# Kernel optimization log

Hardware: AMD Instinct MI355X
Metric: run time of the kernel (lower is better)

The kernel has to match this reference:

```python
import jax, jax.numpy as jnp
import numpy as np

NEG_SLOPE = 0.2


def gatv2_layer(x, edge_index, Wl, Wr, att, bias):
    """PyG GATv2Conv (share_weights=False, concat=True, negative_slope=0.2).
    x: [N, F]; Wl/Wr: [F, H*C]; att: [H, C]; bias: [H*C]. Returns [N, H*C]."""
    N = x.shape[0]
    H, C = att.shape
    src, dst = edge_index[0], edge_index[1]
    xl = (x @ Wl).reshape(N, H, C)  # source transform
    xr = (x @ Wr).reshape(N, H, C)  # target transform
    # per-edge attention logits
    e = jax.nn.leaky_relu(xl[src] + xr[dst], NEG_SLOPE)          # [E, H, C]
    logits = jnp.einsum('ehc,hc->eh', e, att)                     # [E, H]
    # segment softmax over incoming edges of each destination node
    m = jax.ops.segment_max(logits, dst, num_segments=N)          # [N, H]
    m = jnp.where(jnp.isfinite(m), m, 0.0)                        # empty segments
    ex = jnp.exp(logits - m[dst])                                 # [E, H]
    denom = jax.ops.segment_sum(ex, dst, num_segments=N)          # [N, H]
    alpha = ex / (denom[dst] + 1e-16)                             # [E, H]
    msg = xl[src] * alpha[..., None]                              # [E, H, C]
    out = jax.ops.segment_sum(msg, dst, num_segments=N)           # [N, H, C]
    return out.reshape(N, H * C) + bias


def setup_inputs() -> dict:
    key = jax.random.key(0)
    ks = jax.random.split(key, 10)
    N, E, F, H, C, OUT = 50000, 800000, 256, 8, 32, 64
    s = 0.05
    return {
        'x': jax.random.normal(ks[0], (N, F), dtype=jnp.float32),
        'edge_index': jax.random.randint(ks[1], (2, E), 0, N, dtype=jnp.int64),
        'Wl1': jax.random.normal(ks[2], (F, H * C), dtype=jnp.float32) * s,
        'Wr1': jax.random.normal(ks[3], (F, H * C), dtype=jnp.float32) * s,
        'att1': jax.random.normal(ks[4], (H, C), dtype=jnp.float32) * s,
        'b1': jax.random.normal(ks[5], (H * C,), dtype=jnp.float32) * s,
        'Wl2': jax.random.normal(ks[6], (H * C, OUT), dtype=jnp.float32) * s,
        'Wr2': jax.random.normal(ks[7], (H * C, OUT), dtype=jnp.float32) * s,
        'att2': jax.random.normal(ks[8], (1, OUT), dtype=jnp.float32) * s,
        'b2': jax.random.normal(ks[9], (OUT,), dtype=jnp.float32) * s,
    }


def reference(x, edge_index, Wl1, Wr1, att1, b1, Wl2, Wr2, att2, b2):
    h = gatv2_layer(x, edge_index, Wl1, Wr1, att1, b1)
    h = jax.nn.relu(h)
    h = gatv2_layer(h, edge_index, Wl2, Wr2, att2, b2)
    return (h, jax.nn.log_softmax(h, axis=1))
```

## Files before the change

### kernel.cpp

```cpp
#include <hip/hip_runtime.h>
#include <hip/hip_bf16.h>
#include <math.h>

#define NEG_SLOPE 0.2f

typedef __attribute__((ext_vector_type(8))) short short8;
typedef __attribute__((ext_vector_type(4))) float floatx4;
typedef __attribute__((ext_vector_type(2))) float floatx2;

__device__ inline ushort f2b(float f) {
    __hip_bfloat16 b = __float2bfloat16(f);
    return *(ushort*)&b;
}
__device__ inline float b2f(ushort u) {
    union { unsigned int i; float f; } c;
    c.i = ((unsigned int)u) << 16;
    return c.f;
}
__device__ inline floatx2 bf2x2(unsigned int d) {
    union { unsigned int i; float f; } lo, hi;
    lo.i = d << 16;
    hi.i = d & 0xffff0000u;
    floatx2 r = {lo.f, hi.f};
    return r;
}

template<int BM, int BN, typename AT>
__global__ __launch_bounds__(256) void gemm_bf16(const AT* __restrict__ A,
                                                 const ushort* __restrict__ Bt,
                                                 ushort* __restrict__ C,
                                                 int M, int N, int K)
{
    constexpr int SA = 40;
    constexpr int WTM = (BN == 64) ? 32 : 64;
    constexpr int WM  = BM / WTM;
    constexpr int IT  = WTM / 16;
    constexpr int JT  = 4;
    __shared__ ushort As[BM * SA];
    __shared__ ushort Bs[BN * SA];
    const int tid = threadIdx.x;
    const int w = tid >> 6, lane = tid & 63;
    const int mw = (w % WM) * WTM;
    const int nw = (w / WM) * 64;
    const int m0 = blockIdx.y * BM;
    const int n0 = blockIdx.x * BN;
    const int lm = lane & 15;
    const int kg = lane >> 4;

    floatx4 acc[IT][JT];
#pragma unroll
    for (int i = 0; i < IT; ++i)
#pragma unroll
        for (int j = 0; j < JT; ++j) acc[i][j] = (floatx4)0.f;

    for (int k0 = 0; k0 < K; k0 += 32) {
#pragma unroll
        for (int it = 0; it < BM / 64; ++it) {
            int idx = it * 256 + tid;
            int row = idx >> 2, kc = idx & 3;
            int grow = m0 + row;
            if (grow >= M) grow = M - 1;
            if constexpr (sizeof(AT) == 4) {
                float4 f0 = *(const float4*)&A[(size_t)grow * K + k0 + kc * 8];
                float4 f1 = *(const float4*)&A[(size_t)grow * K + k0 + kc * 8 + 4];
                ushort* d = &As[row * SA + kc * 8];
                d[0] = f2b(f0.x); d[1] = f2b(f0.y); d[2] = f2b(f0.z); d[3] = f2b(f0.w);
                d[4] = f2b(f1.x); d[5] = f2b(f1.y); d[6] = f2b(f1.z); d[7] = f2b(f1.w);
            } else {
                short8 v = *(const short8*)&A[(size_t)grow * K + k0 + kc * 8];
                *(short8*)&As[row * SA + kc * 8] = v;
            }
        }
#pragma unroll
        for (int it = 0; it < BN / 64; ++it) {
            int idx = it * 256 + tid;
            int row = idx >> 2, kc = idx & 3;
            short8 v = *(const short8*)&Bt[(size_t)(n0 + row) * K + k0 + kc * 8];
            *(short8*)&Bs[row * SA + kc * 8] = v;
        }
        __syncthreads();
        short8 a[IT], b[JT];
#pragma unroll
        for (int i = 0; i < IT; ++i)
            a[i] = *(const short8*)&As[(mw + i * 16 + lm) * SA + kg * 8];
#pragma unroll
        for (int j = 0; j < JT; ++j)
            b[j] = *(const short8*)&Bs[(nw + j * 16 + lm) * SA + kg * 8];
#pragma unroll
        for (int i = 0; i < IT; ++i)
#pragma unroll
            for (int j = 0; j < JT; ++j)
                acc[i][j] = __builtin_amdgcn_mfma_f32_16x16x32_bf16(a[i], b[j], acc[i][j], 0, 0, 0);
        __syncthreads();
    }

#pragma unroll
    for (int i = 0; i < IT; ++i) {
        int rbase = m0 + mw + i * 16 + (lane >> 4) * 4;
#pragma unroll
        for (int j = 0; j < JT; ++j) {
            int col = n0 + nw + j * 16 + lm;
#pragma unroll
            for (int r = 0; r < 4; ++r) {
                int row = rbase + r;
                if (row < M) C[(size_t)row * N + col] = f2b(acc[i][j][r]);
            }
        }
    }
}

__global__ void k_prep(const float* __restrict__ Wl1, const float* __restrict__ Wr1,
                       const float* __restrict__ Wl2, const float* __restrict__ Wr2,
                       ushort* __restrict__ wlr1t, ushort* __restrict__ wlr2t,
                       const int* __restrict__ dst, int E, int* __restrict__ counts)
{
    const int b = blockIdx.x;
    const int t = threadIdx.x;
    if (b < 640) {
        int i = b * 256 + t;
        if (i < 65536) {
            int k = i >> 8, n = i & 255;
            wlr1t[n * 256 + k] = f2b(Wl1[i]);
        } else if (i < 131072) {
            int j = i - 65536;
            int k = j >> 8, n = j & 255;
            wlr1t[65536 + n * 256 + k] = f2b(Wr1[j]);
        } else if (i < 147456) {
            int j = i - 131072;
            int k = j >> 6, n = j & 63;
            wlr2t[n * 256 + k] = f2b(Wl2[j]);
        } else {
            int j = i - 147456;
            int k = j >> 6, n = j & 63;
            wlr2t[16384 + n * 256 + k] = f2b(Wr2[j]);
        }
    } else {
        int i = (b - 640) * 256 + t;
        if (i < E) atomicAdd(&counts[dst[i]], 1);
    }
}

__global__ void k_chunksum(const int* __restrict__ counts, int N, int* __restrict__ chunk)
{
    __shared__ int sm[256];
    const int t = threadIdx.x;
    const int base = blockIdx.x * 1024;
    int s = 0;
    for (int i = t; i < 1024; i += 256) {
        int idx = base + i;
        s += (idx < N) ? counts[idx] : 0;
    }
    sm[t] = s;
    __syncthreads();
    for (int off = 128; off; off >>= 1) {
        if (t < off) sm[t] += sm[t + off];
        __syncthreads();
    }
    if (t == 0) chunk[blockIdx.x] = sm[0];
}

__global__ void k_scanchunk(int* __restrict__ chunk, int nchunks)
{
    if (blockIdx.x == 0 && threadIdx.x == 0) {
        int run = 0;
        for (int i = 0; i < nchunks; ++i) {
            int c = chunk[i];
            chunk[i] = run;
            run += c;
        }
        chunk[nchunks] = run;
    }
}

__global__ void k_scanwrite(const int* __restrict__ counts, int N,
                            const int* __restrict__ chunk,
                            int* __restrict__ offsets, int* __restrict__ cursor)
{
    __shared__ int sm[256];
    const int t = threadIdx.x;
    const int base = blockIdx.x * 1024 + t * 4;
    int v[4];
    int s = 0;
#pragma unroll
    for (int i = 0; i < 4; ++i) {
        v[i] = (base + i < N) ? counts[base + i] : 0;
        s += v[i];
    }
    sm[t] = s;
    __syncthreads();
    for (int off = 1; off < 256; off <<= 1) {
        int y = (t >= off) ? sm[t - off] : 0;
        __syncthreads();
        sm[t] += y;
        __syncthreads();
    }
    int run = chunk[blockIdx.x] + sm[t] - s;
#pragma unroll
    for (int i = 0; i < 4; ++i) {
        if (base + i < N) {
            offsets[base + i] = run;
            cursor[base + i] = run;
        }
        run += v[i];
    }
    if (blockIdx.x == 0 && t == 0) offsets[N] = chunk[gridDim.x];
}

__global__ void k_fill(const int* __restrict__ src, const int* __restrict__ dst,
                       int E, int* __restrict__ cursor, int* __restrict__ csr_src)
{
    int i = blockIdx.x * blockDim.x + threadIdx.x;
    if (i < E) {
        int d = dst[i];
        int pos = atomicAdd(&cursor[d], 1);
        csr_src[pos] = src[i];
    }
}

__global__ __launch_bounds__(256) void agg1(const ushort* __restrict__ xlr,
                                            const float* __restrict__ att,
                                            const float* __restrict__ bias,
                                            const int* __restrict__ offsets,
                                            const int* __restrict__ csr_src,
                                            ushort* __restrict__ h1, int N)
{
    const int wave = blockIdx.x * 4 + (threadIdx.x >> 6);
    const int lane = threadIdx.x & 63;
    if (wave >= N) return;
    const int n = wave;
    const int g = lane >> 5;
    const int sl = lane & 31;
    const int elem = (sl >> 2) * 32 + (sl & 3) * 8;

    floatx2 attv2[4], xrv2[4];
    {
        uint4 xr8 = *(const uint4*)&xlr[(size_t)n * 512 + 256 + elem];
        unsigned int xw[4] = {xr8.x, xr8.y, xr8.z, xr8.w};
#pragma unroll
        for (int i = 0; i < 4; ++i) {
            attv2[i] = *(const floatx2*)&att[elem + 2 * i];
            xrv2[i] = bf2x2(xw[i]);
        }
    }
    float m = -1e30f, l = 0.f;
    floatx2 acc2[4] = {(floatx2)0.f, (floatx2)0.f, (floatx2)0.f, (floatx2)0.f};

    const int beg = offsets[n], end = offsets[n + 1];
    if (beg < end) {
        uint4 xv;
        {
            int k0 = beg + g;
            int ks = (k0 < end) ? k0 : end - 1;
            xv = *(const uint4*)&xlr[(size_t)csr_src[ks] * 512 + elem];
        }
        for (int kb = beg; kb < end; kb += 2) {
            const int kk = kb + g;
            uint4 cur = xv;
            {
                int kn = kk + 2;
                int ks = (kn < end) ? kn : end - 1;
                xv = *(const uint4*)&xlr[(size_t)csr_src[ks] * 512 + elem];
            }
            if (kk < end) {
                unsigned int cw[4] = {cur.x, cur.y, cur.z, cur.w};
                floatx2 xl2[4];
                floatx2 u2 = (floatx2)0.f;
#pragma unroll
                for (int i = 0; i < 4; ++i) {
                    xl2[i] = bf2x2(cw[i]);
                    floatx2 t = xl2[i] + xrv2[i];
                    t = __builtin_elementwise_max(t, t * NEG_SLOPE);
                    u2 += t * attv2[i];
                }
                float u = u2.x + u2.y;
                u += __shfl_xor(u, 1);
                u += __shfl_xor(u, 2);
                float e = __expf(-fabsf(u - m));
                bool kp = (m >= u);
                float sc = kp ? 1.f : e;
                float p  = kp ? e : 1.f;
                m = fmaxf(m, u);
#pragma unroll
                for (int i = 0; i < 4; ++i) acc2[i] = acc2[i] * sc + xl2[i] * p;
                l = fmaf(l, sc, p);
            }
        }
    }
    {
        float mo = __shfl_xor(m, 32);
        float lo = __shfl_xor(l, 32);
        float nm = fmaxf(m, mo);
        float ea = __expf(m - nm);
        float eb = __expf(mo - nm);
#pragma unroll
        for (int i = 0; i < 4; ++i) {
            floatx2 ao = {__shfl_xor(acc2[i].x, 32), __shfl_xor(acc2[i].y, 32)};
            acc2[i] = acc2[i] * ea + ao * eb;
        }
        l = l * ea + lo * eb;
    }
    if (g == 0) {
        float rl = 1.f / (l + 1e-16f);
        short8 o;
#pragma unroll
        for (int i = 0; i < 4; ++i) {
            float v0 = fmaf(acc2[i].x, rl, bias[elem + 2 * i]);
            float v1 = fmaf(acc2[i].y, rl, bias[elem + 2 * i + 1]);
            o[2 * i]     = (short)f2b(fmaxf(v0, 0.f));
            o[2 * i + 1] = (short)f2b(fmaxf(v1, 0.f));
        }
        *(short8*)&h1[(size_t)n * 256 + elem] = o;
    }
}

__global__ __launch_bounds__(256) void agg2(const ushort* __restrict__ xlr,
                                            const float* __restrict__ att,
                                            const float* __restrict__ bias,
                                            const int* __restrict__ offsets,
                                            const int* __restrict__ csr_src,
                                            float* __restrict__ out, int N)
{
    const int wave = blockIdx.x * 4 + (threadIdx.x >> 6);
    const int lane = threadIdx.x & 63;
    if (wave >= N) return;
    const int n = wave;
    const int g = lane >> 4;
    const int c0 = (lane & 15) * 4;

    floatx2 attv2[2], xrv2[2];
    {
        uint2 xr4 = *(const uint2*)&xlr[(size_t)n * 128 + 64 + c0];
        attv2[0] = *(const floatx2*)&att[c0];
        attv2[1] = *(const floatx2*)&att[c0 + 2];
        xrv2[0] = bf2x2(xr4.x);
        xrv2[1] = bf2x2(xr4.y);
    }
    float m = -1e30f, l = 0.f;
    floatx2 acc2[2] = {(floatx2)0.f, (floatx2)0.f};

    const int beg = offsets[n], end = offsets[n + 1];
    if (beg < end) {
        uint2 xv;
        {
            int k0 = beg + g;
            int ks = (k0 < end) ? k0 : end - 1;
            xv = *(const uint2*)&xlr[(size_t)csr_src[ks] * 128 + c0];
        }
        for (int kb = beg; kb < end; kb += 4) {
            const int kk = kb + g;
            uint2 cur = xv;
            {
                int kn = kk + 4;
                int ks = (kn < end) ? kn : end - 1;
                xv = *(const uint2*)&xlr[(size_t)csr_src[ks] * 128 + c0];
            }
            if (kk < end) {
                floatx2 xl2[2];
                xl2[0] = bf2x2(cur.x);
                xl2[1] = bf2x2(cur.y);
                floatx2 u2 = (floatx2)0.f;
#pragma unroll
                for (int i = 0; i < 2; ++i) {
                    floatx2 t = xl2[i] + xrv2[i];
                    t = __builtin_elementwise_max(t, t * NEG_SLOPE);
                    u2 += t * attv2[i];
                }
                float u = u2.x + u2.y;
                u += __shfl_xor(u, 1);
                u += __shfl_xor(u, 2);
                u += __shfl_xor(u, 4);
                u += __shfl_xor(u, 8);
                float e = __expf(-fabsf(u - m));
                bool kp = (m >= u);
                float sc = kp ? 1.f : e;
                float p  = kp ? e : 1.f;
                m = fmaxf(m, u);
#pragma unroll
                for (int i = 0; i < 2; ++i) acc2[i] = acc2[i] * sc + xl2[i] * p;
                l = fmaf(l, sc, p);
            }
        }
    }
#pragma unroll
    for (int off = 16; off <= 32; off <<= 1) {
        float mo = __shfl_xor(m, off);
        float lo = __shfl_xor(l, off);
        float nm = fmaxf(m, mo);
        float sa = __expf(m - nm);
        float sb = __expf(mo - nm);
#pragma unroll
        for (int i = 0; i < 2; ++i) {
            floatx2 ao = {__shfl_xor(acc2[i].x, off), __shfl_xor(acc2[i].y, off)};
            acc2[i] = acc2[i] * sa + ao * sb;
        }
        l = l * sa + lo * sb;
        m = nm;
    }
    float rl = 1.f / (l + 1e-16f);
    float h[4];
    h[0] = acc2[0].x * rl + bias[c0];
    h[1] = acc2[0].y * rl + bias[c0 + 1];
    h[2] = acc2[1].x * rl + bias[c0 + 2];
    h[3] = acc2[1].y * rl + bias[c0 + 3];

    float mx = fmaxf(fmaxf(h[0], h[1]), fmaxf(h[2], h[3]));
    mx = fmaxf(mx, __shfl_xor(mx, 1));
    mx = fmaxf(mx, __shfl_xor(mx, 2));
    mx = fmaxf(mx, __shfl_xor(mx, 4));
    mx = fmaxf(mx, __shfl_xor(mx, 8));
    float ssum = __expf(h[0] - mx) + __expf(h[1] - mx) + __expf(h[2] - mx) + __expf(h[3] - mx);
    ssum += __shfl_xor(ssum, 1);
    ssum += __shfl_xor(ssum, 2);
    ssum += __shfl_xor(ssum, 4);
    ssum += __shfl_xor(ssum, 8);
    float lg = __logf(ssum);
    if (g == 0) {
        float4 o1 = make_float4(h[0], h[1], h[2], h[3]);
        *(float4*)&out[(size_t)n * 64 + c0] = o1;
        float4 o2 = make_float4(h[0] - mx - lg, h[1] - mx - lg, h[2] - mx - lg, h[3] - mx - lg);
        *(float4*)&out[(size_t)(N + n) * 64 + c0] = o2;
    }
}

extern "C" void kernel_launch(void* const* d_in, const int* in_sizes, int n_in,
                              void* d_out, int out_size, void* d_ws, size_t ws_size,
                              hipStream_t stream)
{
    const float* x    = (const float*)d_in[0];
    const int*   ei   = (const int*)d_in[1];
    const float* Wl1  = (const float*)d_in[2];
    const float* Wr1  = (const float*)d_in[3];
    const float* att1 = (const float*)d_in[4];
    const float* b1   = (const float*)d_in[5];
    const float* Wl2  = (const float*)d_in[6];
    const float* Wr2  = (const float*)d_in[7];
    const float* att2 = (const float*)d_in[8];
    const float* b2   = (const float*)d_in[9];
    float* out = (float*)d_out;

    const int F = 256;
    const int E = in_sizes[1] / 2;
    const int N = in_sizes[0] / F;

    const int* e_src = ei;
    const int* e_dst = ei + E;

    ushort* wlr1t = (ushort*)d_ws;
    ushort* wlr2t = wlr1t + 512 * 256;
    ushort* xlr1  = wlr2t + 128 * 256;
    ushort* h1b   = xlr1 + (size_t)N * 512;
    ushort* xlr2  = h1b + (size_t)N * 256;
    int* offsets  = (int*)(xlr2 + (size_t)N * 128);
    int* cursor   = offsets + (N + 1);
    int* counts   = cursor + (N + 1);
    int* chunkoff = counts + N;
    int* csr_src  = chunkoff + 66;

    const int nchunks = (N + 1023) / 1024;

    hipMemsetAsync(counts, 0, (size_t)N * sizeof(int), stream);
    k_prep<<<640 + (E + 255) / 256, 256, 0, stream>>>(Wl1, Wr1, Wl2, Wr2,
                                                      wlr1t, wlr2t, e_dst, E, counts);

    gemm_bf16<128, 128, float><<<dim3(4, (N + 127) / 128), 256, 0, stream>>>(x, wlr1t, xlr1, N, 512, F);

    k_chunksum<<<nchunks, 256, 0, stream>>>(counts, N, chunkoff);
    k_scanchunk<<<1, 64, 0, stream>>>(chunkoff, nchunks);
    k_scanwrite<<<nchunks, 256, 0, stream>>>(counts, N, chunkoff, offsets, cursor);
    k_fill<<<(E + 255) / 256, 256, 0, stream>>>(e_src, e_dst, E, cursor, csr_src);

    agg1<<<(N + 3) / 4, 256, 0, stream>>>(xlr1, att1, b1, offsets, csr_src, h1b, N);

    gemm_bf16<128, 64, ushort><<<dim3(2, (N + 127) / 128), 256, 0, stream>>>(h1b, wlr2t, xlr2, N, 128, 256);
    agg2<<<(N + 3) / 4, 256, 0, stream>>>(xlr2, att2, b2, offsets, csr_src, out, N);
}
```

Baseline: 358.1 us.

## Pre-convert x to bf16, store byte offsets in CSR, deepen gather prefetch

```diff
diff --git a/kernel.cpp b/kernel.cpp
--- a/kernel.cpp
+++ b/kernel.cpp
@@ -11,11 +11,6 @@
 __device__ inline ushort f2b(float f) {
     __hip_bfloat16 b = __float2bfloat16(f);
     return *(ushort*)&b;
-}
-__device__ inline float b2f(ushort u) {
-    union { unsigned int i; float f; } c;
-    c.i = ((unsigned int)u) << 16;
-    return c.f;
 }
 __device__ inline floatx2 bf2x2(unsigned int d) {
     union { unsigned int i; float f; } lo, hi;
@@ -25,8 +20,8 @@
     return r;
 }
 
-template<int BM, int BN, typename AT>
-__global__ __launch_bounds__(256) void gemm_bf16(const AT* __restrict__ A,
+template<int BM, int BN>
+__global__ __launch_bounds__(256) void gemm_bf16(const ushort* __restrict__ A,
                                                  const ushort* __restrict__ Bt,
                                                  ushort* __restrict__ C,
                                                  int M, int N, int K)
@@ -60,16 +55,8 @@
             int row = idx >> 2, kc = idx & 3;
             int grow = m0 + row;
             if (grow >= M) grow = M - 1;
-            if constexpr (sizeof(AT) == 4) {
-                float4 f0 = *(const float4*)&A[(size_t)grow * K + k0 + kc * 8];
-                float4 f1 = *(const float4*)&A[(size_t)grow * K + k0 + kc * 8 + 4];
-                ushort* d = &As[row * SA + kc * 8];
-                d[0] = f2b(f0.x); d[1] = f2b(f0.y); d[2] = f2b(f0.z); d[3] = f2b(f0.w);
-                d[4] = f2b(f1.x); d[5] = f2b(f1.y); d[6] = f2b(f1.z); d[7] = f2b(f1.w);
-            } else {
-                short8 v = *(const short8*)&A[(size_t)grow * K + k0 + kc * 8];
-                *(short8*)&As[row * SA + kc * 8] = v;
-            }
+            short8 v = *(const short8*)&A[(size_t)grow * K + k0 + kc * 8];
+            *(short8*)&As[row * SA + kc * 8] = v;
         }
 #pragma unroll
         for (int it = 0; it < BN / 64; ++it) {
@@ -109,15 +96,26 @@
     }
 }
 
-__global__ void k_prep(const float* __restrict__ Wl1, const float* __restrict__ Wr1,
+__global__ void k_prep(const float* __restrict__ x, ushort* __restrict__ xb, int XB,
+                       const float* __restrict__ Wl1, const float* __restrict__ Wr1,
                        const float* __restrict__ Wl2, const float* __restrict__ Wr2,
                        ushort* __restrict__ wlr1t, ushort* __restrict__ wlr2t,
                        const int* __restrict__ dst, int E, int* __restrict__ counts)
 {
     const int b = blockIdx.x;
     const int t = threadIdx.x;
-    if (b < 640) {
-        int i = b * 256 + t;
+    if (b < XB) {
+        int i = b * 2048 + t * 8;
+        float4 f0 = *(const float4*)&x[i];
+        float4 f1 = *(const float4*)&x[i + 4];
+        short8 o;
+        o[0] = (short)f2b(f0.x); o[1] = (short)f2b(f0.y);
+        o[2] = (short)f2b(f0.z); o[3] = (short)f2b(f0.w);
+        o[4] = (short)f2b(f1.x); o[5] = (short)f2b(f1.y);
+        o[6] = (short)f2b(f1.z); o[7] = (short)f2b(f1.w);
+        *(short8*)&xb[i] = o;
+    } else if (b < XB + 640) {
+        int i = (b - XB) * 256 + t;
         if (i < 65536) {
             int k = i >> 8, n = i & 255;
             wlr1t[n * 256 + k] = f2b(Wl1[i]);
@@ -135,7 +133,7 @@
             wlr2t[16384 + n * 256 + k] = f2b(Wr2[j]);
         }
     } else {
-        int i = (b - 640) * 256 + t;
+        int i = (b - XB - 640) * 256 + t;
         if (i < E) atomicAdd(&counts[dst[i]], 1);
     }
 }
@@ -161,15 +159,16 @@
 
 __global__ void k_scanchunk(int* __restrict__ chunk, int nchunks)
 {
-    if (blockIdx.x == 0 && threadIdx.x == 0) {
-        int run = 0;
-        for (int i = 0; i < nchunks; ++i) {
-            int c = chunk[i];
-            chunk[i] = run;
-            run += c;
-        }
-        chunk[nchunks] = run;
-    }
+    const int t = threadIdx.x;
+    int v = (t < nchunks) ? chunk[t] : 0;
+    int inc = v;
+#pragma unroll
+    for (int off = 1; off < 64; off <<= 1) {
+        int y = __shfl_up(inc, off);
+        if (t >= off) inc += y;
+    }
+    if (t < nchunks) chunk[t] = inc - v;
+    if (t == nchunks - 1) chunk[nchunks] = inc;
 }
 
 __global__ void k_scanwrite(const int* __restrict__ counts, int N,
@@ -207,13 +206,13 @@
 }
 
 __global__ void k_fill(const int* __restrict__ src, const int* __restrict__ dst,
-                       int E, int* __restrict__ cursor, int* __restrict__ csr_src)
+                       int E, int* __restrict__ cursor, int* __restrict__ csr_off)
 {
     int i = blockIdx.x * blockDim.x + threadIdx.x;
     if (i < E) {
         int d = dst[i];
         int pos = atomicAdd(&cursor[d], 1);
-        csr_src[pos] = src[i];
+        csr_off[pos] = src[i] * 1024;
     }
 }
 
@@ -221,7 +220,7 @@
                                             const float* __restrict__ att,
                                             const float* __restrict__ bias,
                                             const int* __restrict__ offsets,
-                                            const int* __restrict__ csr_src,
+                                            const int* __restrict__ csr_off,
                                             ushort* __restrict__ h1, int N)
 {
     const int wave = blockIdx.x * 4 + (threadIdx.x >> 6);
@@ -231,10 +230,12 @@
     const int g = lane >> 5;
     const int sl = lane & 31;
     const int elem = (sl >> 2) * 32 + (sl & 3) * 8;
+    const char* __restrict__ xbase = (const char*)xlr;
+    const int ebyte = elem * 2;
 
     floatx2 attv2[4], xrv2[4];
     {
-        uint4 xr8 = *(const uint4*)&xlr[(size_t)n * 512 + 256 + elem];
+        uint4 xr8 = *(const uint4*)(xbase + (size_t)n * 1024 + 512 + ebyte);
         unsigned int xw[4] = {xr8.x, xr8.y, xr8.z, xr8.w};
 #pragma unroll
         for (int i = 0; i < 4; ++i) {
@@ -246,45 +247,41 @@
     floatx2 acc2[4] = {(floatx2)0.f, (floatx2)0.f, (floatx2)0.f, (floatx2)0.f};
 
     const int beg = offsets[n], end = offsets[n + 1];
-    if (beg < end) {
-        uint4 xv;
-        {
-            int k0 = beg + g;
-            int ks = (k0 < end) ? k0 : end - 1;
-            xv = *(const uint4*)&xlr[(size_t)csr_src[ks] * 512 + elem];
-        }
-        for (int kb = beg; kb < end; kb += 2) {
-            const int kk = kb + g;
-            uint4 cur = xv;
-            {
-                int kn = kk + 2;
-                int ks = (kn < end) ? kn : end - 1;
-                xv = *(const uint4*)&xlr[(size_t)csr_src[ks] * 512 + elem];
-            }
-            if (kk < end) {
-                unsigned int cw[4] = {cur.x, cur.y, cur.z, cur.w};
-                floatx2 xl2[4];
-                floatx2 u2 = (floatx2)0.f;
-#pragma unroll
-                for (int i = 0; i < 4; ++i) {
-                    xl2[i] = bf2x2(cw[i]);
-                    floatx2 t = xl2[i] + xrv2[i];
-                    t = __builtin_elementwise_max(t, t * NEG_SLOPE);
-                    u2 += t * attv2[i];
-                }
-                float u = u2.x + u2.y;
-                u += __shfl_xor(u, 1);
-                u += __shfl_xor(u, 2);
-                float e = __expf(-fabsf(u - m));
-                bool kp = (m >= u);
-                float sc = kp ? 1.f : e;
-                float p  = kp ? e : 1.f;
-                m = fmaxf(m, u);
-#pragma unroll
-                for (int i = 0; i < 4; ++i) acc2[i] = acc2[i] * sc + xl2[i] * p;
-                l = fmaf(l, sc, p);
-            }
-        }
+    uint4 vA, vB;
+    int oC;
+    {
+        int k0 = beg + g;
+        if (k0 < end) vA = *(const uint4*)(xbase + (unsigned)csr_off[k0] + ebyte);
+        if (k0 + 2 < end) vB = *(const uint4*)(xbase + (unsigned)csr_off[k0 + 2] + ebyte);
+        if (k0 + 4 < end) oC = csr_off[k0 + 4];
+    }
+    for (int kk = beg + g; kk < end; kk += 2) {
+        uint4 cur = vA;
+        vA = vB;
+        if (kk + 4 < end) vB = *(const uint4*)(xbase + (unsigned)oC + ebyte);
+        if (kk + 6 < end) oC = csr_off[kk + 6];
+
+        unsigned int cw[4] = {cur.x, cur.y, cur.z, cur.w};
+        floatx2 xl2[4];
+        floatx2 u2 = (floatx2)0.f;
+#pragma unroll
+        for (int i = 0; i < 4; ++i) {
+            xl2[i] = bf2x2(cw[i]);
+            floatx2 t = xl2[i] + xrv2[i];
+            t = __builtin_elementwise_max(t, t * NEG_SLOPE);
+            u2 += t * attv2[i];
+        }
+        float u = u2.x + u2.y;
+        u += __shfl_xor(u, 1);
+        u += __shfl_xor(u, 2);
+        float e = __expf(-fabsf(u - m));
+        bool kp = (m >= u);
+        float sc = kp ? 1.f : e;
+        float p  = kp ? e : 1.f;
+        m = fmaxf(m, u);
+#pragma unroll
+        for (int i = 0; i < 4; ++i) acc2[i] = acc2[i] * sc + xl2[i] * p;
+        l = fmaf(l, sc, p);
     }
     {
         float mo = __shfl_xor(m, 32);
@@ -317,7 +314,7 @@
                                             const float* __restrict__ att,
                                             const float* __restrict__ bias,
                                             const int* __restrict__ offsets,
-                                            const int* __restrict__ csr_src,
+                                            const int* __restrict__ csr_off,
                                             float* __restrict__ out, int N)
 {
     const int wave = blockIdx.x * 4 + (threadIdx.x >> 6);
@@ -326,10 +323,12 @@
     const int n = wave;
     const int g = lane >> 4;
     const int c0 = (lane & 15) * 4;
+    const char* __restrict__ xbase = (const char*)xlr;
+    const int cbyte = c0 * 2;
 
     floatx2 attv2[2], xrv2[2];
     {
-        uint2 xr4 = *(const uint2*)&xlr[(size_t)n * 128 + 64 + c0];
+        uint2 xr4 = *(const uint2*)(xbase + (size_t)n * 256 + 128 + cbyte);
         attv2[0] = *(const floatx2*)&att[c0];
         attv2[1] = *(const floatx2*)&att[c0 + 2];
         xrv2[0] = bf2x2(xr4.x);
@@ -339,47 +338,43 @@
     floatx2 acc2[2] = {(floatx2)0.f, (floatx2)0.f};
 
     const int beg = offsets[n], end = offsets[n + 1];
-    if (beg < end) {
-        uint2 xv;
-        {
-            int k0 = beg + g;
-            int ks = (k0 < end) ? k0 : end - 1;
-            xv = *(const uint2*)&xlr[(size_t)csr_src[ks] * 128 + c0];
-        }
-        for (int kb = beg; kb < end; kb += 4) {
-            const int kk = kb + g;
-            uint2 cur = xv;
-            {
-                int kn = kk + 4;
-                int ks = (kn < end) ? kn : end - 1;
-                xv = *(const uint2*)&xlr[(size_t)csr_src[ks] * 128 + c0];
-            }
-            if (kk < end) {
-                floatx2 xl2[2];
-                xl2[0] = bf2x2(cur.x);
-                xl2[1] = bf2x2(cur.y);
-                floatx2 u2 = (floatx2)0.f;
-#pragma unroll
-                for (int i = 0; i < 2; ++i) {
-                    floatx2 t = xl2[i] + xrv2[i];
-                    t = __builtin_elementwise_max(t, t * NEG_SLOPE);
-                    u2 += t * attv2[i];
-                }
-                float u = u2.x + u2.y;
-                u += __shfl_xor(u, 1);
-                u += __shfl_xor(u, 2);
-                u += __shfl_xor(u, 4);
-                u += __shfl_xor(u, 8);
-                float e = __expf(-fabsf(u - m));
-                bool kp = (m >= u);
-                float sc = kp ? 1.f : e;
-                float p  = kp ? e : 1.f;
-                m = fmaxf(m, u);
-#pragma unroll
-                for (int i = 0; i < 2; ++i) acc2[i] = acc2[i] * sc + xl2[i] * p;
-                l = fmaf(l, sc, p);
-            }
-        }
+    uint2 vA, vB;
+    int oC;
+    {
+        int k0 = beg + g;
+        if (k0 < end) vA = *(const uint2*)(xbase + ((unsigned)csr_off[k0] >> 2) + cbyte);
+        if (k0 + 4 < end) vB = *(const uint2*)(xbase + ((unsigned)csr_off[k0 + 4] >> 2) + cbyte);
+        if (k0 + 8 < end) oC = csr_off[k0 + 8];
+    }
+    for (int kk = beg + g; kk < end; kk += 4) {
+        uint2 cur = vA;
+        vA = vB;
+        if (kk + 8 < end) vB = *(const uint2*)(xbase + ((unsigned)oC >> 2) + cbyte);
+        if (kk + 12 < end) oC = csr_off[kk + 12];
+
+        floatx2 xl2[2];
+        xl2[0] = bf2x2(cur.x);
+        xl2[1] = bf2x2(cur.y);
+        floatx2 u2 = (floatx2)0.f;
+#pragma unroll
+        for (int i = 0; i < 2; ++i) {
+            floatx2 t = xl2[i] + xrv2[i];
+            t = __builtin_elementwise_max(t, t * NEG_SLOPE);
+            u2 += t * attv2[i];
+        }
+        float u = u2.x + u2.y;
+        u += __shfl_xor(u, 1);
+        u += __shfl_xor(u, 2);
+        u += __shfl_xor(u, 4);
+        u += __shfl_xor(u, 8);
+        float e = __expf(-fabsf(u - m));
+        bool kp = (m >= u);
+        float sc = kp ? 1.f : e;
+        float p  = kp ? e : 1.f;
+        m = fmaxf(m, u);
+#pragma unroll
+        for (int i = 0; i < 2; ++i) acc2[i] = acc2[i] * sc + xl2[i] * p;
+        l = fmaf(l, sc, p);
     }
 #pragma unroll
     for (int off = 16; off <= 32; off <<= 1) {
@@ -445,7 +440,8 @@
     const int* e_src = ei;
     const int* e_dst = ei + E;
 
-    ushort* wlr1t = (ushort*)d_ws;
+    ushort* xb    = (ushort*)d_ws;
+    ushort* wlr1t = xb + (size_t)N * 256;
     ushort* wlr2t = wlr1t + 512 * 256;
     ushort* xlr1  = wlr2t + 128 * 256;
     ushort* h1b   = xlr1 + (size_t)N * 512;
@@ -454,23 +450,24 @@
     int* cursor   = offsets + (N + 1);
     int* counts   = cursor + (N + 1);
     int* chunkoff = counts + N;
-    int* csr_src  = chunkoff + 66;
+    int* csr_off  = chunkoff + 66;
 
     const int nchunks = (N + 1023) / 1024;
+    const int XB = (N * 256) / 2048;
 
     hipMemsetAsync(counts, 0, (size_t)N * sizeof(int), stream);
-    k_prep<<<640 + (E + 255) / 256, 256, 0, stream>>>(Wl1, Wr1, Wl2, Wr2,
-                                                      wlr1t, wlr2t, e_dst, E, counts);
-
-    gemm_bf16<128, 128, float><<<dim3(4, (N + 127) / 128), 256, 0, stream>>>(x, wlr1t, xlr1, N, 512, F);
+    k_prep<<<XB + 640 + (E + 255) / 256, 256, 0, stream>>>(
+        x, xb, XB, Wl1, Wr1, Wl2, Wr2, wlr1t, wlr2t, e_dst, E, counts);
+
+    gemm_bf16<128, 128><<<dim3(4, (N + 127) / 128), 256, 0, stream>>>(xb, wlr1t, xlr1, N, 512, F);
 
     k_chunksum<<<nchunks, 256, 0, stream>>>(counts, N, chunkoff);
     k_scanchunk<<<1, 64, 0, stream>>>(chunkoff, nchunks);
     k_scanwrite<<<nchunks, 256, 0, stream>>>(counts, N, chunkoff, offsets, cursor);
-    k_fill<<<(E + 255) / 256, 256, 0, stream>>>(e_src, e_dst, E, cursor, csr_src);
-
-    agg1<<<(N + 3) / 4, 256, 0, stream>>>(xlr1, att1, b1, offsets, csr_src, h1b, N);
-
-    gemm_bf16<128, 64, ushort><<<dim3(2, (N + 127) / 128), 256, 0, stream>>>(h1b, wlr2t, xlr2, N, 128, 256);
-    agg2<<<(N + 3) / 4, 256, 0, stream>>>(xlr2, att2, b2, offsets, csr_src, out, N);
-}
+    k_fill<<<(E + 255) / 256, 256, 0, stream>>>(e_src, e_dst, E, cursor, csr_off);
+
+    agg1<<<(N + 3) / 4, 256, 0, stream>>>(xlr1, att1, b1, offsets, csr_off, h1b, N);
+
+    gemm_bf16<128, 64><<<dim3(2, (N + 127) / 128), 256, 0, stream>>>(h1b, wlr2t, xlr2, N, 128, 256);
+    agg2<<<(N + 3) / 4, 256, 0, stream>>>(xlr2, att2, b2, offsets, csr_off, out, N);
+}
```

Measured after the change: 340.5 us. 4.9% less time.
